# Performance work log

Hardware: AMD Instinct MI355X
Metric: run time of the kernel (lower is better)

## Reference

```python
import jax, jax.numpy as jnp
import numpy as np
import math

D_MODEL = 768
N_HEADS = 6
HD = D_MODEL // N_HEADS  # 128
RANK = D_MODEL // 4      # 192
B, T = 128, 256


def _rope_tables(T, dim):
    # matches torch: inv = 1/10000**(arange(0,dim,2)/dim); emb = cat([outer(t,inv)]*2, -1)
    inv = 1.0 / (10000.0 ** (jnp.arange(0, dim, 2, dtype=jnp.float32) / dim))
    t = jnp.arange(T, dtype=jnp.float32)
    freqs = jnp.outer(t, inv)                       # [T, dim/2]
    emb = jnp.concatenate([freqs, freqs], axis=-1)  # [T, dim]
    return jnp.cos(emb), jnp.sin(emb)               # each [T, dim]


def _rot(x):
    h = x.shape[-1] // 2
    return jnp.concatenate([-x[..., h:], x[..., :h]], axis=-1)


def setup_inputs() -> dict:
    key = jax.random.key(0)
    ks = jax.random.split(key, 8)
    s_in = 1.0 / math.sqrt(D_MODEL)
    s_r = 1.0 / math.sqrt(RANK)
    inp = {
        'x': jax.random.normal(ks[0], (B, T, D_MODEL), dtype=jnp.float32),
        'qA': jax.random.normal(ks[1], (D_MODEL, RANK), dtype=jnp.float32) * s_in,
        'qB': jax.random.normal(ks[2], (RANK, D_MODEL), dtype=jnp.float32) * s_r,
        'kA': jax.random.normal(ks[3], (D_MODEL, RANK), dtype=jnp.float32) * s_in,
        'kB': jax.random.normal(ks[4], (RANK, D_MODEL), dtype=jnp.float32) * s_r,
        'vA': jax.random.normal(ks[5], (D_MODEL, RANK), dtype=jnp.float32) * s_in,
        'vB': jax.random.normal(ks[6], (RANK, D_MODEL), dtype=jnp.float32) * s_r,
        'o_w': jax.random.normal(ks[7], (D_MODEL, D_MODEL), dtype=jnp.float32) * s_in,
    }
    return inp


def reference(x, qA, qB, kA, kB, vA, vB, o_w):
    Bb, Tt, _ = x.shape
    # low-rank projections: in -> rank -> out, then split heads [B, H, T, hd]
    def proj(A, W):
        h = (x @ A) @ W
        return h.reshape(Bb, Tt, N_HEADS, HD).transpose(0, 2, 1, 3)
    q = proj(qA, qB)
    k = proj(kA, kB)
    v = proj(vA, vB)
    cos, sin = _rope_tables(Tt, HD)  # [T, hd], broadcast over B, H
    q = q * cos + _rot(q) * sin
    k = k * cos + _rot(k) * sin
    att = jnp.einsum('bhqd,bhkd->bhqk', q, k) / math.sqrt(HD)
    causal = jnp.tril(jnp.ones((Tt, Tt), dtype=bool))
    att = jnp.where(causal, att, -jnp.inf)
    att = jax.nn.softmax(att, axis=-1)
    out = jnp.einsum('bhqk,bhkd->bhqd', att, v)          # [B, H, T, hd]
    out = out.transpose(0, 2, 1, 3).reshape(Bb, Tt, D_MODEL)
    return out @ o_w
```

## Files before the change

### kernel.cpp

```cpp
#include <hip/hip_runtime.h>
#include <hip/hip_bf16.h>
#include <stdint.h>

typedef __attribute__((ext_vector_type(8))) short s16x8;
typedef __attribute__((ext_vector_type(4))) float f32x4;

#define D_MODEL 768
#define N_HEADS 6
#define HD 128
#define RANK 192
#define TT 256
#define NROW 32768
#define QKV_LD 2304
#define NK 12
#define QSCL 0.08838834764831845f

__device__ inline short f2bf(float f) {
  union { float f; unsigned u; } x; x.f = f;
  unsigned r = x.u + 0x7fffu + ((x.u >> 16) & 1u);
  return (short)(r >> 16);
}
__device__ inline float bf2f(short v) {
  union { unsigned u; float f; } x; x.u = ((unsigned)(unsigned short)v) << 16;
  return x.f;
}
__device__ inline void gload_lds16(const void* g, void* lds) {
  __builtin_amdgcn_global_load_lds(
      (const __attribute__((address_space(1))) unsigned int*)g,
      (__attribute__((address_space(3))) unsigned int*)lds, 16, 0, 0);
}

#define BAR()    asm volatile("s_barrier" ::: "memory")
#define LGKM0()  asm volatile("s_waitcnt lgkmcnt(0)" ::: "memory")
#define WAITVM4() asm volatile("s_waitcnt vmcnt(4)" ::: "memory")
#define WAITVM0() asm volatile("s_waitcnt vmcnt(0)" ::: "memory")

__global__ void k_tables(float* __restrict__ cosT, float* __restrict__ sinT) {
  int tid = blockIdx.x * 256 + threadIdx.x;
  int t = tid >> 6, i = tid & 63;
  float inv = powf(10000.0f, -(float)i / 64.0f);
  float ang = (float)t * inv;
  cosT[tid] = cosf(ang);
  sinT[tid] = sinf(ang);
}

__global__ void k_castx(const float* __restrict__ x, short* __restrict__ xb) {
  int t = blockIdx.x * 256 + threadIdx.x;
  const float4* xp = (const float4*)x;
  float4 a = xp[t * 2], b = xp[t * 2 + 1];
  s16x8 o;
  o[0] = f2bf(a.x); o[1] = f2bf(a.y); o[2] = f2bf(a.z); o[3] = f2bf(a.w);
  o[4] = f2bf(b.x); o[5] = f2bf(b.y); o[6] = f2bf(b.z); o[7] = f2bf(b.w);
  *(s16x8*)(xb + (size_t)t * 8) = o;
}

__global__ void k_makew(const float* __restrict__ qA, const float* __restrict__ qB,
                        const float* __restrict__ kA, const float* __restrict__ kB,
                        const float* __restrict__ vA, const float* __restrict__ vB,
                        short* __restrict__ WT) {
  int g = blockIdx.x * 256 + threadIdx.x;
  int n4 = g % 576, kkb = g / 576;
  int part = n4 / 192, nnb = (n4 % 192) * 4;
  const float* A = (part == 0) ? qA : (part == 1) ? kA : vA;
  const float* Bm = (part == 0) ? qB : (part == 1) ? kB : vB;
  float acc[4][4] = {};
  for (int r0 = 0; r0 < RANK; r0 += 4) {
    float4 a4[4], b4[4];
#pragma unroll
    for (int q = 0; q < 4; ++q)
      a4[q] = *(const float4*)&A[(kkb + q * 192) * RANK + r0];
#pragma unroll
    for (int i = 0; i < 4; ++i)
      b4[i] = *(const float4*)&Bm[(r0 + i) * 768 + nnb];
#pragma unroll
    for (int q = 0; q < 4; ++q) {
      const float* aq = (const float*)&a4[q];
#pragma unroll
      for (int i = 0; i < 4; ++i) {
        const float* bi = (const float*)&b4[i];
#pragma unroll
        for (int jn = 0; jn < 4; ++jn)
          acc[q][jn] += aq[i] * bi[jn];
      }
    }
  }
#pragma unroll
  for (int q = 0; q < 4; ++q)
#pragma unroll
    for (int jn = 0; jn < 4; ++jn)
      WT[(size_t)(part * 768 + nnb + jn) * 768 + kkb + q * 192] = f2bf(acc[q][jn]);
}

__global__ void k_wot(const float* __restrict__ ow, short* __restrict__ WT) {
  int g = blockIdx.x * 256 + threadIdx.x;
  int n = g % 768, kk = g / 768;
  WT[(size_t)(2304 + n) * 768 + kk] = f2bf(ow[(size_t)kk * 768 + n]);
}

__device__ inline s16x8 rdfrag(const short* hbase, int rowbyte, int ksl4x, int swz) {
  return *(const s16x8*)((const char*)hbase + rowbyte + (((ksl4x) ^ (swz)) << 4));
}

template <bool OUTBF>
__global__ __launch_bounds__(512, 2) void k_gemm8(const short* __restrict__ A,
                                                  const short* __restrict__ Bt,
                                                  void* __restrict__ Cv, int ldc) {
  extern __shared__ short lds[];
  const int tid = threadIdx.x;
  const int wid = tid >> 6, lane = tid & 63;
  const int l15 = lane & 15, l4 = lane >> 4;
  const int wr = wid >> 2, wc = wid & 3;
  const int swz = l15 & 7;
  const int bid = blockIdx.y * 128 + blockIdx.x;
  const int nper = gridDim.y;
  const int xcd = bid & 7, loc = bid >> 3;
  const int mq = loc / nper;
  const int mt = xcd * 16 + mq;
  const int nt = loc - mq * nper;
  const long mbase = (long)mt * 256;
  const long nbase = (long)nt * 256;

  const int hb0 = wid * 2048 + lane * 16;
  const int hb1 = hb0 + 1024;
  const int r0 = hb0 >> 7, c0 = ((hb0 >> 4) & 7) ^ (r0 & 7);
  const int r1 = hb1 >> 7, c1 = ((hb1 >> 4) & 7) ^ (r1 & 7);
  const int off0 = r0 * 768 + c0 * 8;
  const int off1 = r1 * 768 + c1 * 8;

#define STAGE(G, rowoff, kt, ldsS) do {                                        \
    gload_lds16((G) + (size_t)(rowoff) * 768 + (kt) * 64 + off0,               \
                (char*)(ldsS) + wid * 2048);                                   \
    gload_lds16((G) + (size_t)(rowoff) * 768 + (kt) * 64 + off1,               \
                (char*)(ldsS) + wid * 2048 + 1024);                            \
  } while (0)

#define LDSA(buf, half) (lds + ((buf) * 2 + (half)) * 8192)
#define LDSB(buf, half) (lds + 32768 + ((buf) * 2 + (half)) * 8192)

  f32x4 acc[8][4] = {};

  STAGE(A,  mbase,       0, LDSA(0, 0));
  STAGE(Bt, nbase,       0, LDSB(0, 0));
  STAGE(A,  mbase + 128, 0, LDSA(0, 1));
  STAGE(Bt, nbase + 128, 0, LDSB(0, 1));
  STAGE(A,  mbase,       1, LDSA(1, 0));
  STAGE(Bt, nbase,       1, LDSB(1, 0));
  WAITVM4();
  BAR();

  s16x8 a03[4][2], a47[4][2], b01[2][2], b23[2][2];

#pragma unroll
  for (int kt = 0; kt < NK; ++kt) {
    const int buf = kt & 1, nbuf = buf ^ 1;
    const short* Ab = LDSA(buf, wr);
    const short* Bb = LDSB(buf, (wc >> 1));
    const int browbase = (wc & 1) * 64 * 128;

#pragma unroll
    for (int mf = 0; mf < 4; ++mf)
#pragma unroll
      for (int ks = 0; ks < 2; ++ks)
        a03[mf][ks] = rdfrag(Ab, (mf * 16 + l15) * 128, ks * 4 + l4, swz);
#pragma unroll
    for (int nf = 0; nf < 2; ++nf)
#pragma unroll
      for (int ks = 0; ks < 2; ++ks)
        b01[nf][ks] = rdfrag(Bb, browbase + (nf * 16 + l15) * 128, ks * 4 + l4, swz);
    if (kt + 1 < NK) STAGE(A, mbase + 128, kt + 1, LDSA(nbuf, 1));
    BAR();
    LGKM0();
    __builtin_amdgcn_s_setprio(1);
#pragma unroll
    for (int mf = 0; mf < 4; ++mf)
#pragma unroll
      for (int nf = 0; nf < 2; ++nf)
#pragma unroll
        for (int ks = 0; ks < 2; ++ks)
          acc[mf][nf] = __builtin_amdgcn_mfma_f32_16x16x32_bf16(a03[mf][ks], b01[nf][ks], acc[mf][nf], 0, 0, 0);
    __builtin_amdgcn_s_setprio(0);
    BAR();

#pragma unroll
    for (int mf = 0; mf < 4; ++mf)
#pragma unroll
      for (int ks = 0; ks < 2; ++ks)
        a47[mf][ks] = rdfrag(Ab, ((mf + 4) * 16 + l15) * 128, ks * 4 + l4, swz);
    if (kt + 1 < NK) STAGE(Bt, nbase + 128, kt + 1, LDSB(nbuf, 1));
    BAR();
    LGKM0();
    __builtin_amdgcn_s_setprio(1);
#pragma unroll
    for (int mf = 0; mf < 4; ++mf)
#pragma unroll
      for (int nf = 0; nf < 2; ++nf)
#pragma unroll
        for (int ks = 0; ks < 2; ++ks)
          acc[mf + 4][nf] = __builtin_amdgcn_mfma_f32_16x16x32_bf16(a47[mf][ks], b01[nf][ks], acc[mf + 4][nf], 0, 0, 0);
    __builtin_amdgcn_s_setprio(0);
    BAR();

#pragma unroll
    for (int nf = 0; nf < 2; ++nf)
#pragma unroll
      for (int ks = 0; ks < 2; ++ks)
        b23[nf][ks] = rdfrag(Bb, browbase + ((nf + 2) * 16 + l15) * 128, ks * 4 + l4, swz);
    if (kt + 2 < NK) STAGE(A, mbase, kt + 2, LDSA(buf, 0));
    BAR();
    LGKM0();
    __builtin_amdgcn_s_setprio(1);
#pragma unroll
    for (int mf = 0; mf < 4; ++mf)
#pragma unroll
      for (int nf = 0; nf < 2; ++nf)
#pragma unroll
        for (int ks = 0; ks < 2; ++ks)
          acc[mf][nf + 2] = __builtin_amdgcn_mfma_f32_16x16x32_bf16(a03[mf][ks], b23[nf][ks], acc[mf][nf + 2], 0, 0, 0);
    __builtin_amdgcn_s_setprio(0);
    BAR();

    if (kt + 2 < NK) STAGE(Bt, nbase, kt + 2, LDSB(buf, 0));
    BAR();
    __builtin_amdgcn_s_setprio(1);
#pragma unroll
    for (int mf = 0; mf < 4; ++mf)
#pragma unroll
      for (int nf = 0; nf < 2; ++nf)
#pragma unroll
        for (int ks = 0; ks < 2; ++ks)
          acc[mf + 4][nf + 2] = __builtin_amdgcn_mfma_f32_16x16x32_bf16(a47[mf][ks], b23[nf][ks], acc[mf + 4][nf + 2], 0, 0, 0);
    __builtin_amdgcn_s_setprio(0);
    if (kt < NK - 1) {
      if (kt + 2 < NK) WAITVM4(); else WAITVM0();
      BAR();
    }
  }
#undef STAGE

#pragma unroll
  for (int mf = 0; mf < 8; ++mf)
#pragma unroll
    for (int nf = 0; nf < 4; ++nf)
#pragma unroll
      for (int r = 0; r < 4; ++r) {
        long row = mbase + wr * 128 + mf * 16 + l4 * 4 + r;
        long col = nbase + wc * 64 + nf * 16 + l15;
        if (OUTBF) ((short*)Cv)[row * ldc + col] = f2bf(acc[mf][nf][r]);
        else       ((float*)Cv)[row * ldc + col] = acc[mf][nf][r];
      }
}

__global__ void k_ropek(short* __restrict__ qkv, const float* __restrict__ cosT,
                        const float* __restrict__ sinT) {
  int tid = blockIdx.x * 256 + threadIdx.x;
  int row = tid / 48, rem = tid % 48;
  int head = rem >> 3, i8 = (rem & 7) * 8;
  int t = row & (TT - 1);
  size_t base = (size_t)row * QKV_LD + D_MODEL + head * 128 + i8;
  s16x8 a = *(const s16x8*)(qkv + base);
  s16x8 b = *(const s16x8*)(qkv + base + 64);
  const float4* cp = (const float4*)(cosT + t * 64 + i8);
  const float4* sp = (const float4*)(sinT + t * 64 + i8);
  float4 c04 = cp[0], c14 = cp[1], s04 = sp[0], s14 = sp[1];
  float cs[8] = {c04.x, c04.y, c04.z, c04.w, c14.x, c14.y, c14.z, c14.w};
  float sn[8] = {s04.x, s04.y, s04.z, s04.w, s14.x, s14.y, s14.z, s14.w};
  s16x8 na, nb;
#pragma unroll
  for (int j = 0; j < 8; ++j) {
    float av = bf2f(a[j]), bv = bf2f(b[j]);
    na[j] = f2bf(av * cs[j] - bv * sn[j]);
    nb[j] = f2bf(bv * cs[j] + av * sn[j]);
  }
  *(s16x8*)(qkv + base) = na;
  *(s16x8*)(qkv + base + 64) = nb;
}

__global__ __launch_bounds__(512) void k_attn(const short* __restrict__ qkv,
                                              short* __restrict__ attout,
                                              const float* __restrict__ cosT,
                                              const float* __restrict__ sinT) {
  extern __shared__ short smem[];
  short* Kls0 = smem;
  short* Kls1 = smem + 8192;
  short* Vt   = smem + 16384;
  short* PlsW;
  const int tid = threadIdx.x;
  const int wid = tid >> 6, lane = tid & 63;
  const int l15 = lane & 15, l4 = lane >> 4;
  PlsW = smem + 24576 + wid * 2048;
  const int b = blockIdx.x / N_HEADS, h = blockIdx.x % N_HEADS;
  const long row0 = (long)b * TT;
  const int d0 = wid * 16;

  s16x8 qf[2][4];
#pragma unroll
  for (int mi = 0; mi < 2; ++mi)
#pragma unroll
    for (int kc = 0; kc < 4; ++kc) {
      long row = row0 + wid * 32 + mi * 16 + l15;
      qf[mi][kc] = *(const s16x8*)(qkv + row * QKV_LD + h * HD + kc * 32 + l4 * 8);
    }
#pragma unroll
  for (int mi = 0; mi < 2; ++mi) {
    int t = wid * 32 + mi * 16 + l15;
#pragma unroll
    for (int kc = 0; kc < 2; ++kc) {
      const float4* cp = (const float4*)(cosT + t * 64 + kc * 32 + l4 * 8);
      const float4* sp = (const float4*)(sinT + t * 64 + kc * 32 + l4 * 8);
      float4 c04 = cp[0], c14 = cp[1], s04 = sp[0], s14 = sp[1];
      float cs[8] = {c04.x, c04.y, c04.z, c04.w, c14.x, c14.y, c14.z, c14.w};
      float sn[8] = {s04.x, s04.y, s04.z, s04.w, s14.x, s14.y, s14.z, s14.w};
#pragma unroll
      for (int jj = 0; jj < 8; ++jj) {
        float av = bf2f(qf[mi][kc][jj]);
        float bv = bf2f(qf[mi][kc + 2][jj]);
        qf[mi][kc][jj]     = f2bf((av * cs[jj] - bv * sn[jj]) * QSCL);
        qf[mi][kc + 2][jj] = f2bf((bv * cs[jj] + av * sn[jj]) * QSCL);
      }
    }
  }

#define STAGEK(j_, Kd) do {                                                     \
    int bb0_ = wid * 2048 + lane * 16;                                          \
    int r0_ = bb0_ >> 8; int sc0_ = ((bb0_ >> 4) & 15) ^ (r0_ & 7);             \
    gload_lds16(qkv + (row0 + (j_) * 64 + r0_) * QKV_LD + D_MODEL + h * HD + sc0_ * 8, \
                (char*)(Kd) + wid * 2048);                                      \
    int bb1_ = bb0_ + 1024;                                                     \
    int r1_ = bb1_ >> 8; int sc1_ = ((bb1_ >> 4) & 15) ^ (r1_ & 7);             \
    gload_lds16(qkv + (row0 + (j_) * 64 + r1_) * QKV_LD + D_MODEL + h * HD + sc1_ * 8, \
                (char*)(Kd) + wid * 2048 + 1024);                               \
  } while (0)

#define LOADV(j_, va, vb) do {                                                  \
    const short* vsrc_ = qkv + (row0 + (j_) * 64 + lane) * QKV_LD + 2 * D_MODEL + h * HD + d0; \
    va = *(const s16x8*)vsrc_;                                                  \
    vb = *(const s16x8*)(vsrc_ + 8);                                            \
  } while (0)

  float mst[2][4], lst[2][4];
  f32x4 oacc[2][8];
#pragma unroll
  for (int mi = 0; mi < 2; ++mi)
#pragma unroll
    for (int r = 0; r < 4; ++r) { mst[mi][r] = -1e30f; lst[mi][r] = 0.f; }
#pragma unroll
  for (int mi = 0; mi < 2; ++mi)
#pragma unroll
    for (int nd = 0; nd < 8; ++nd) oacc[mi][nd] = {0.f, 0.f, 0.f, 0.f};

  const int jmax = (wid * 32 + 31) / 64;

  STAGEK(0, Kls0);
  s16x8 vr[2][2];
  LOADV(0, vr[0][0], vr[0][1]);

#pragma unroll
  for (int j = 0; j < 4; ++j) {
    const int buf = j & 1;
    const short* Kb = buf ? Kls1 : Kls0;
    short* Kn = buf ? Kls0 : Kls1;
    if (j < 3) {
      STAGEK(j + 1, Kn);
      LOADV(j + 1, vr[buf ^ 1][0], vr[buf ^ 1][1]);
    }
    if (j < 3) WAITVM4(); else WAITVM0();
    __builtin_amdgcn_sched_barrier(0);
    BAR();
#pragma unroll
    for (int e = 0; e < 8; ++e)
      *(short*)((char*)Vt + (d0 + e) * 128 + (((lane >> 3) ^ e) << 4) + (lane & 7) * 2) = vr[buf][0][e];
#pragma unroll
    for (int e = 0; e < 8; ++e)
      *(short*)((char*)Vt + (d0 + 8 + e) * 128 + (((lane >> 3) ^ e) << 4) + (lane & 7) * 2) = vr[buf][1][e];

    if (j <= jmax) {
      f32x4 sacc[2][4] = {};
#pragma unroll
      for (int kc = 0; kc < 4; ++kc) {
        s16x8 kf[4];
#pragma unroll
        for (int ni = 0; ni < 4; ++ni)
          kf[ni] = *(const s16x8*)((const char*)Kb + (ni * 16 + l15) * 256 +
                                   (((kc * 4 + l4) ^ (l15 & 7)) << 4));
#pragma unroll
        for (int mi = 0; mi < 2; ++mi)
#pragma unroll
          for (int ni = 0; ni < 4; ++ni)
            sacc[mi][ni] = __builtin_amdgcn_mfma_f32_16x16x32_bf16(qf[mi][kc], kf[ni], sacc[mi][ni], 0, 0, 0);
      }
#pragma unroll
      for (int mi = 0; mi < 2; ++mi) {
#pragma unroll
        for (int r = 0; r < 4; ++r) {
          int qr = wid * 32 + mi * 16 + l4 * 4 + r;
          float rm = -1e30f;
#pragma unroll
          for (int ni = 0; ni < 4; ++ni) {
            int kvc = j * 64 + ni * 16 + l15;
            if (kvc > qr) sacc[mi][ni][r] = -1e30f;
            rm = fmaxf(rm, sacc[mi][ni][r]);
          }
#pragma unroll
          for (int d2 = 1; d2 < 16; d2 <<= 1)
            rm = fmaxf(rm, __shfl_xor(rm, d2, 64));
          float mold = mst[mi][r];
          float mnew = fmaxf(mold, rm);
          float alpha = __expf(mold - mnew);
          mst[mi][r] = mnew;
          float rs = 0.f;
#pragma unroll
          for (int ni = 0; ni < 4; ++ni) {
            float p = __expf(sacc[mi][ni][r] - mnew);
            sacc[mi][ni][r] = p;
            rs += p;
          }
#pragma unroll
          for (int d2 = 1; d2 < 16; d2 <<= 1)
            rs += __shfl_xor(rs, d2, 64);
          lst[mi][r] = lst[mi][r] * alpha + rs;
#pragma unroll
          for (int nd = 0; nd < 8; ++nd)
            oacc[mi][nd][r] *= alpha;
        }
      }
#pragma unroll
      for (int mi = 0; mi < 2; ++mi)
#pragma unroll
        for (int ni = 0; ni < 4; ++ni)
#pragma unroll
          for (int r = 0; r < 4; ++r) {
            int prow = mi * 16 + l4 * 4 + r;
            int pcp = (ni * 2 + (l15 >> 3)) ^ (prow & 7);
            *(short*)((char*)PlsW + prow * 128 + (pcp << 4) + (l15 & 7) * 2) =
                f2bf(sacc[mi][ni][r]);
          }
    }
    LGKM0();
    BAR();
    __builtin_amdgcn_sched_barrier(0);
    if (j <= jmax) {
#pragma unroll
      for (int kc2 = 0; kc2 < 2; ++kc2) {
        s16x8 pa[2];
#pragma unroll
        for (int mi = 0; mi < 2; ++mi)
          pa[mi] = *(const s16x8*)((const char*)PlsW + (mi * 16 + l15) * 128 +
                                   (((kc2 * 4 + l4) ^ (l15 & 7)) << 4));
#pragma unroll
        for (int nd = 0; nd < 8; ++nd) {
          s16x8 vf = *(const s16x8*)((const char*)Vt + (nd * 16 + l15) * 128 +
                                     (((kc2 * 4 + l4) ^ (l15 & 7)) << 4));
#pragma unroll
          for (int mi = 0; mi < 2; ++mi)
            oacc[mi][nd] = __builtin_amdgcn_mfma_f32_16x16x32_bf16(pa[mi], vf, oacc[mi][nd], 0, 0, 0);
        }
      }
    }
  }
#undef STAGEK
#undef LOADV
#pragma unroll
  for (int mi = 0; mi < 2; ++mi)
#pragma unroll
    for (int nd = 0; nd < 8; ++nd)
#pragma unroll
      for (int r = 0; r < 4; ++r) {
        long row = row0 + wid * 32 + mi * 16 + l4 * 4 + r;
        int col = h * HD + nd * 16 + l15;
        attout[row * D_MODEL + col] = f2bf(oacc[mi][nd][r] / lst[mi][r]);
      }
}

extern "C" void kernel_launch(void* const* d_in, const int* in_sizes, int n_in,
                              void* d_out, int out_size, void* d_ws, size_t ws_size,
                              hipStream_t stream) {
  const float* x  = (const float*)d_in[0];
  const float* qA = (const float*)d_in[1];
  const float* qB = (const float*)d_in[2];
  const float* kA = (const float*)d_in[3];
  const float* kB = (const float*)d_in[4];
  const float* vA = (const float*)d_in[5];
  const float* vB = (const float*)d_in[6];
  const float* ow = (const float*)d_in[7];

  char* ws = (char*)d_ws;
  short* qkv   = (short*)ws;
  short* xb    = (short*)(ws + 150994944);
  short* WT    = (short*)(ws + 201326592);
  float* cosT  = (float*)(ws + 206045184);
  float* sinT  = (float*)(ws + 206110720);
  short* attout = xb;

  hipFuncSetAttribute((const void*)k_gemm8<true>,
                      hipFuncAttributeMaxDynamicSharedMemorySize, 131072);
  hipFuncSetAttribute((const void*)k_gemm8<false>,
                      hipFuncAttributeMaxDynamicSharedMemorySize, 131072);
  hipFuncSetAttribute((const void*)k_attn,
                      hipFuncAttributeMaxDynamicSharedMemorySize, 81920);

  k_tables<<<64, 256, 0, stream>>>(cosT, sinT);
  k_castx<<<12288, 256, 0, stream>>>(x, xb);
  k_makew<<<432, 256, 0, stream>>>(qA, qB, kA, kB, vA, vB, WT);
  k_wot<<<2304, 256, 0, stream>>>(ow, WT);
  k_gemm8<true><<<dim3(128, 9), 512, 131072, stream>>>(xb, WT, (void*)qkv, QKV_LD);
  k_ropek<<<6144, 256, 0, stream>>>(qkv, cosT, sinT);
  k_attn<<<768, 512, 81920, stream>>>(qkv, attout, cosT, sinT);
  k_gemm8<false><<<dim3(128, 3), 512, 131072, stream>>>(attout, WT + (size_t)2304 * 768, d_out, 768);
}
```

Before: 357.7 us.

## Fuse setup kernels into one launch and balance causal rows across warps

Merges the x cast, output-weight transpose, low-rank weight product and RoPE table kernels into a single launch that dispatches on block index. This removes several launch gaps. In attention, each warp now takes one early and one late 16-row query block (wid and 15-wid), to even out causal work between warps. The key-tile loop bound is adjusted to match, and the change risks extra per-iteration branching on mixed row blocks.

```diff
diff --git a/kernel.cpp b/kernel.cpp
--- a/kernel.cpp
+++ b/kernel.cpp
@@ -35,66 +35,71 @@
 #define WAITVM4() asm volatile("s_waitcnt vmcnt(4)" ::: "memory")
 #define WAITVM0() asm volatile("s_waitcnt vmcnt(0)" ::: "memory")
 
-__global__ void k_tables(float* __restrict__ cosT, float* __restrict__ sinT) {
-  int tid = blockIdx.x * 256 + threadIdx.x;
-  int t = tid >> 6, i = tid & 63;
-  float inv = powf(10000.0f, -(float)i / 64.0f);
-  float ang = (float)t * inv;
-  cosT[tid] = cosf(ang);
-  sinT[tid] = sinf(ang);
-}
-
-__global__ void k_castx(const float* __restrict__ x, short* __restrict__ xb) {
-  int t = blockIdx.x * 256 + threadIdx.x;
-  const float4* xp = (const float4*)x;
-  float4 a = xp[t * 2], b = xp[t * 2 + 1];
-  s16x8 o;
-  o[0] = f2bf(a.x); o[1] = f2bf(a.y); o[2] = f2bf(a.z); o[3] = f2bf(a.w);
-  o[4] = f2bf(b.x); o[5] = f2bf(b.y); o[6] = f2bf(b.z); o[7] = f2bf(b.w);
-  *(s16x8*)(xb + (size_t)t * 8) = o;
-}
-
-__global__ void k_makew(const float* __restrict__ qA, const float* __restrict__ qB,
+#define NB_CAST 12288
+#define NB_WOT  2304
+#define NB_MAKEW 432
+#define NB_TAB  64
+
+__global__ void k_setup(const float* __restrict__ x, short* __restrict__ xb,
+                        const float* __restrict__ ow,
+                        const float* __restrict__ qA, const float* __restrict__ qB,
                         const float* __restrict__ kA, const float* __restrict__ kB,
                         const float* __restrict__ vA, const float* __restrict__ vB,
-                        short* __restrict__ WT) {
-  int g = blockIdx.x * 256 + threadIdx.x;
-  int n4 = g % 576, kkb = g / 576;
-  int part = n4 / 192, nnb = (n4 % 192) * 4;
-  const float* A = (part == 0) ? qA : (part == 1) ? kA : vA;
-  const float* Bm = (part == 0) ? qB : (part == 1) ? kB : vB;
-  float acc[4][4] = {};
-  for (int r0 = 0; r0 < RANK; r0 += 4) {
-    float4 a4[4], b4[4];
+                        short* __restrict__ WT,
+                        float* __restrict__ cosT, float* __restrict__ sinT) {
+  const int bid = blockIdx.x, tid = threadIdx.x;
+  if (bid < NB_CAST) {
+    int t = bid * 256 + tid;
+    const float4* xp = (const float4*)x;
+    float4 a = xp[t * 2], b = xp[t * 2 + 1];
+    s16x8 o;
+    o[0] = f2bf(a.x); o[1] = f2bf(a.y); o[2] = f2bf(a.z); o[3] = f2bf(a.w);
+    o[4] = f2bf(b.x); o[5] = f2bf(b.y); o[6] = f2bf(b.z); o[7] = f2bf(b.w);
+    *(s16x8*)(xb + (size_t)t * 8) = o;
+  } else if (bid < NB_CAST + NB_WOT) {
+    int g = (bid - NB_CAST) * 256 + tid;
+    int n = g % 768, kk = g / 768;
+    WT[(size_t)(2304 + n) * 768 + kk] = f2bf(ow[(size_t)kk * 768 + n]);
+  } else if (bid < NB_CAST + NB_WOT + NB_MAKEW) {
+    int g = (bid - NB_CAST - NB_WOT) * 256 + tid;
+    int n4 = g % 576, kkb = g / 576;
+    int part = n4 / 192, nnb = (n4 % 192) * 4;
+    const float* A = (part == 0) ? qA : (part == 1) ? kA : vA;
+    const float* Bm = (part == 0) ? qB : (part == 1) ? kB : vB;
+    float acc[4][4] = {};
+    for (int r0 = 0; r0 < RANK; r0 += 4) {
+      float4 a4[4], b4[4];
+#pragma unroll
+      for (int q = 0; q < 4; ++q)
+        a4[q] = *(const float4*)&A[(kkb + q * 192) * RANK + r0];
+#pragma unroll
+      for (int i = 0; i < 4; ++i)
+        b4[i] = *(const float4*)&Bm[(r0 + i) * 768 + nnb];
+#pragma unroll
+      for (int q = 0; q < 4; ++q) {
+        const float* aq = (const float*)&a4[q];
+#pragma unroll
+        for (int i = 0; i < 4; ++i) {
+          const float* bi = (const float*)&b4[i];
+#pragma unroll
+          for (int jn = 0; jn < 4; ++jn)
+            acc[q][jn] += aq[i] * bi[jn];
+        }
+      }
+    }
 #pragma unroll
     for (int q = 0; q < 4; ++q)
-      a4[q] = *(const float4*)&A[(kkb + q * 192) * RANK + r0];
-#pragma unroll
-    for (int i = 0; i < 4; ++i)
-      b4[i] = *(const float4*)&Bm[(r0 + i) * 768 + nnb];
-#pragma unroll
-    for (int q = 0; q < 4; ++q) {
-      const float* aq = (const float*)&a4[q];
-#pragma unroll
-      for (int i = 0; i < 4; ++i) {
-        const float* bi = (const float*)&b4[i];
-#pragma unroll
-        for (int jn = 0; jn < 4; ++jn)
-          acc[q][jn] += aq[i] * bi[jn];
-      }
-    }
+#pragma unroll
+      for (int jn = 0; jn < 4; ++jn)
+        WT[(size_t)(part * 768 + nnb + jn) * 768 + kkb + q * 192] = f2bf(acc[q][jn]);
+  } else {
+    int t2 = (bid - NB_CAST - NB_WOT - NB_MAKEW) * 256 + tid;
+    int t = t2 >> 6, i = t2 & 63;
+    float inv = powf(10000.0f, -(float)i / 64.0f);
+    float ang = (float)t * inv;
+    cosT[t2] = cosf(ang);
+    sinT[t2] = sinf(ang);
   }
-#pragma unroll
-  for (int q = 0; q < 4; ++q)
-#pragma unroll
-    for (int jn = 0; jn < 4; ++jn)
-      WT[(size_t)(part * 768 + nnb + jn) * 768 + kkb + q * 192] = f2bf(acc[q][jn]);
-}
-
-__global__ void k_wot(const float* __restrict__ ow, short* __restrict__ WT) {
-  int g = blockIdx.x * 256 + threadIdx.x;
-  int n = g % 768, kk = g / 768;
-  WT[(size_t)(2304 + n) * 768 + kk] = f2bf(ow[(size_t)kk * 768 + n]);
 }
 
 __device__ inline s16x8 rdfrag(const short* hbase, int rowbyte, int ksl4x, int swz) {
@@ -283,26 +288,26 @@
   short* Kls0 = smem;
   short* Kls1 = smem + 8192;
   short* Vt   = smem + 16384;
-  short* PlsW;
   const int tid = threadIdx.x;
   const int wid = tid >> 6, lane = tid & 63;
   const int l15 = lane & 15, l4 = lane >> 4;
-  PlsW = smem + 24576 + wid * 2048;
+  short* PlsW = smem + 24576 + wid * 2048;
   const int b = blockIdx.x / N_HEADS, h = blockIdx.x % N_HEADS;
   const long row0 = (long)b * TT;
   const int d0 = wid * 16;
+  const int rb[2] = {wid, 15 - wid};
 
   s16x8 qf[2][4];
 #pragma unroll
   for (int mi = 0; mi < 2; ++mi)
 #pragma unroll
     for (int kc = 0; kc < 4; ++kc) {
-      long row = row0 + wid * 32 + mi * 16 + l15;
+      long row = row0 + rb[mi] * 16 + l15;
       qf[mi][kc] = *(const s16x8*)(qkv + row * QKV_LD + h * HD + kc * 32 + l4 * 8);
     }
 #pragma unroll
   for (int mi = 0; mi < 2; ++mi) {
-    int t = wid * 32 + mi * 16 + l15;
+    int t = rb[mi] * 16 + l15;
 #pragma unroll
     for (int kc = 0; kc < 2; ++kc) {
       const float4* cp = (const float4*)(cosT + t * 64 + kc * 32 + l4 * 8);
@@ -348,7 +353,7 @@
 #pragma unroll
     for (int nd = 0; nd < 8; ++nd) oacc[mi][nd] = {0.f, 0.f, 0.f, 0.f};
 
-  const int jmax = (wid * 32 + 31) / 64;
+  const int jmax = (15 - wid) >> 2;
 
   STAGEK(0, Kls0);
   s16x8 vr[2][2];
@@ -392,7 +397,7 @@
       for (int mi = 0; mi < 2; ++mi) {
 #pragma unroll
         for (int r = 0; r < 4; ++r) {
-          int qr = wid * 32 + mi * 16 + l4 * 4 + r;
+          int qr = rb[mi] * 16 + l4 * 4 + r;
           float rm = -1e30f;
 #pragma unroll
           for (int ni = 0; ni < 4; ++ni) {
@@ -465,7 +470,7 @@
     for (int nd = 0; nd < 8; ++nd)
 #pragma unroll
       for (int r = 0; r < 4; ++r) {
-        long row = row0 + wid * 32 + mi * 16 + l4 * 4 + r;
+        long row = row0 + rb[mi] * 16 + l4 * 4 + r;
         int col = h * HD + nd * 16 + l15;
         attout[row * D_MODEL + col] = f2bf(oacc[mi][nd][r] / lst[mi][r]);
       }
@@ -498,10 +503,8 @@
   hipFuncSetAttribute((const void*)k_attn,
                       hipFuncAttributeMaxDynamicSharedMemorySize, 81920);
 
-  k_tables<<<64, 256, 0, stream>>>(cosT, sinT);
-  k_castx<<<12288, 256, 0, stream>>>(x, xb);
-  k_makew<<<432, 256, 0, stream>>>(qA, qB, kA, kB, vA, vB, WT);
-  k_wot<<<2304, 256, 0, stream>>>(ow, WT);
+  k_setup<<<NB_CAST + NB_WOT + NB_MAKEW + NB_TAB, 256, 0, stream>>>(
+      x, xb, ow, qA, qB, kA, kB, vA, vB, WT, cosT, sinT);
   k_gemm8<true><<<dim3(128, 9), 512, 131072, stream>>>(xb, WT, (void*)qkv, QKV_LD);
   k_ropek<<<6144, 256, 0, stream>>>(qkv, cosT, sinT);
   k_attn<<<768, 512, 81920, stream>>>(qkv, attout, cosT, sinT);
```

Result: slower. 384.1 us (+7.4%).
